# Optimization experiments

Measured on AMD Instinct MI355X. Metric: run time of the kernel, lower is better.

## Reference

```python
import jax, jax.numpy as jnp
import numpy as np
from jax import lax

# dims
BATCH, SEQ, DMODEL = 2, 2048, 1024
EXPAND, HEADDIM, DSTATE, DCONV, MLP_INNER = 2, 64, 64, 4, 4096
DIN = EXPAND * DMODEL            # 2048
NH = DIN // HEADDIM              # 32 heads
CONV_DIM = DIN + 2 * DSTATE      # x, B, C go through the depthwise conv
DPROJ = 2 * DIN + 2 * DSTATE + NH  # z, xBC, dt
EPS = 1e-5


def rmsnorm(x, w):
    return x * lax.rsqrt(jnp.mean(x * x, axis=-1, keepdims=True) + EPS) * w


def setup_inputs() -> dict:
    key = jax.random.key(0)
    ks = jax.random.split(key, 12)
    n = lambda i, shape, scale: jax.random.normal(ks[i], shape, jnp.float32) * scale
    return {
        "hidden_tokens": n(0, (BATCH, SEQ, DMODEL), 1.0),
        "W_in": n(1, (DMODEL, DPROJ), DMODEL ** -0.5),
        "conv_w": n(2, (CONV_DIM, DCONV), 0.2),
        "conv_b": jnp.zeros((CONV_DIM,), jnp.float32),
        "dt_bias": jax.random.uniform(ks[3], (NH,), jnp.float32, -4.0, -1.0),
        "A_log": jnp.log(jax.random.uniform(ks[4], (NH,), jnp.float32, 1.0, 16.0)),
        "D_param": n(5, (NH,), 1.0),
        "norm_w": jnp.ones((DIN,), jnp.float32),
        "W_out": n(6, (DIN, DMODEL), DIN ** -0.5),
        "rms_w": jnp.ones((DMODEL,), jnp.float32),
        "mlp_w1": n(7, (DMODEL, MLP_INNER), DMODEL ** -0.5),
        "mlp_b1": jnp.zeros((MLP_INNER,), jnp.float32),
        "mlp_w2": n(8, (MLP_INNER, DMODEL), MLP_INNER ** -0.5),
        "mlp_b2": jnp.zeros((DMODEL,), jnp.float32),
    }


def _mamba2(x, W_in, conv_w, conv_b, dt_bias, A_log, D_param, norm_w, W_out):
    b, l, _ = x.shape
    zxbcdt = x @ W_in                                   # (b,l,DPROJ)
    z = zxbcdt[..., :DIN]
    xBC = zxbcdt[..., DIN:DIN + CONV_DIM]
    dt = zxbcdt[..., DIN + CONV_DIM:]                   # (b,l,NH)

    # depthwise causal conv1d over sequence
    xt = jnp.pad(xBC, ((0, 0), (DCONV - 1, 0), (0, 0))).transpose(0, 2, 1)  # (b,c,l+pad)
    conv = lax.conv_general_dilated(xt, conv_w[:, None, :], (1,), "VALID",
                                    feature_group_count=CONV_DIM,
                                    dimension_numbers=("NCH", "OIH", "NCH"))
    xBC = jax.nn.silu(conv.transpose(0, 2, 1) + conv_b)  # (b,l,CONV_DIM)

    xs = xBC[..., :DIN].reshape(b, l, NH, HEADDIM)       # (b,l,h,p)
    Bc = xBC[..., DIN:DIN + DSTATE]                      # (b,l,n), ngroups=1
    Cc = xBC[..., DIN + DSTATE:]                         # (b,l,n)

    dt = jax.nn.softplus(dt + dt_bias)                   # (b,l,h)
    A = -jnp.exp(A_log)                                  # (h,)
    dA = jnp.exp(dt * A)                                 # (b,l,h)
    dtx = dt[..., None] * xs                             # (b,l,h,p)

    def step(h, inp):
        dA_t, dtx_t, B_t, C_t = inp                      # (b,h),(b,h,p),(b,n),(b,n)
        h = dA_t[..., None, None] * h + dtx_t[..., None] * B_t[:, None, None, :]
        y = jnp.einsum("bhpn,bn->bhp", h, C_t)
        return h, y

    h0 = jnp.zeros((b, NH, HEADDIM, DSTATE), x.dtype)
    _, ys = lax.scan(step, h0, (dA.transpose(1, 0, 2), dtx.transpose(1, 0, 2, 3),
                                Bc.transpose(1, 0, 2), Cc.transpose(1, 0, 2)))
    y = ys.transpose(1, 0, 2, 3) + D_param[None, None, :, None] * xs  # (b,l,h,p)
    y = y.reshape(b, l, DIN)
    y = rmsnorm(y * jax.nn.silu(z), norm_w)              # gated RMSNorm
    return y @ W_out


def reference(hidden_tokens, W_in, conv_w, conv_b, dt_bias, A_log, D_param,
              norm_w, W_out, rms_w, mlp_w1, mlp_b1, mlp_w2, mlp_b2):
    h = hidden_tokens + _mamba2(hidden_tokens, W_in, conv_w, conv_b, dt_bias,
                                A_log, D_param, norm_w, W_out)
    hn = rmsnorm(h, rms_w)
    mlp = jax.nn.silu(hn @ mlp_w1 + mlp_b1) @ mlp_w2 + mlp_b2
    return h + mlp
```

## Files before the change

kernel.cpp:

```cpp
#include <hip/hip_runtime.h>
#include <hip/hip_bf16.h>
#include <cstdint>
#include <cstddef>

#define BATCH 2
#define SEQ 2048
#define DMODEL 1024
#define DIN 2048
#define NH 32
#define HEADDIM 64
#define DSTATE 64
#define DCONV 4
#define CONV_DIM (DIN + 2 * DSTATE)
#define DPROJ (2 * DIN + 2 * DSTATE + NH)
#define MLP_INNER 4096
#define TOKENS (BATCH * SEQ)
#define EPS 1e-5f
#define Q 64
#define NCHUNK (SEQ / Q)
#define NCH (BATCH * NCHUNK * NH)
#define LSTR 72
#define NPAD_IN 4352

typedef __attribute__((ext_vector_type(8))) short short8;
typedef __attribute__((ext_vector_type(8))) __bf16 bf16x8;
typedef __attribute__((ext_vector_type(4))) float f32x4;

__device__ inline short f2bf(float f) {
    unsigned u = __builtin_bit_cast(unsigned, f);
    u = (u + 0x7FFFu + ((u >> 16) & 1u)) >> 16;
    return (short)u;
}
__device__ inline float bf2f(short s) {
    unsigned u = ((unsigned)(unsigned short)s) << 16;
    return __builtin_bit_cast(float, u);
}
__device__ inline float silu_f(float x) { return x / (1.f + __expf(-x)); }

__device__ inline bf16x8 ld_frag(const short* p) {
    short8 s = *(const short8*)p;
    return __builtin_bit_cast(bf16x8, s);
}

__device__ inline void glds16(const short* g, short* l) {
    __builtin_amdgcn_global_load_lds(
        (const __attribute__((address_space(1))) void*)g,
        (__attribute__((address_space(3))) void*)l, 16, 0, 0);
}

template <int MODE>
__global__ __launch_bounds__(512, 2) void gemm256_kernel(
    const short* __restrict__ A, const short* __restrict__ BT,
    void* __restrict__ Cout, const float* __restrict__ bias,
    int M, int N, int K)
{
    const int tid  = threadIdx.x;
    const int wid  = tid >> 6;
    const int lane = tid & 63;
    const int lm   = lane & 15;
    const int lg   = lane >> 4;
    const int wm   = (wid >> 2) * 128;
    const int wn   = (wid & 3) * 64;

    const int nb  = gridDim.x * gridDim.y;
    const int bid = blockIdx.y * gridDim.x + blockIdx.x;
    const int per = nb >> 3;
    const int nid = (bid & 7) * per + (bid >> 3);
    const int m0  = (nid / gridDim.x) * 256;
    const int n0  = (nid % gridDim.x) * 256;

    __shared__ __attribute__((aligned(16))) short Ab[2][2][256 * 32];
    __shared__ __attribute__((aligned(16))) short Bb[2][2][256 * 32];

    f32x4 acc[8][4];
#pragma unroll
    for (int i = 0; i < 8; ++i)
#pragma unroll
        for (int j = 0; j < 4; ++j) acc[i][j] = {0.f, 0.f, 0.f, 0.f};

    const int q   = tid & 7;
    const int jj  = (tid >> 3) & 3;
    const int win = tid >> 5;
    const int r0  = win * 8 + q;
    const short* Asrc = A  + (size_t)(m0 + r0) * K + jj * 8;
    const short* Bsrc = BT + (size_t)(n0 + r0) * K + jj * 8;
    const size_t rstep = (size_t)128 * K;
    const int dst = wid * 512;

#define STAGE(src, buf) do {                  \
        glds16((src), (buf) + dst);           \
        glds16((src) + rstep, (buf) + 4096 + dst); } while (0)

    bf16x8 af[8], bfr[4];

#define READ_A(As, i0, i1) do {                                                \
        _Pragma("unroll")                                                      \
        for (int fi = (i0); fi < (i1); ++fi) {                                 \
            int rr = wm + fi * 16 + lm;                                        \
            af[fi] = ld_frag((As) + ((rr >> 3) << 8) + ((rr & 7) << 3) + (lg << 6)); \
        }                                                                      \
    } while (0)

#define READ_B(Bs, j0, j1) do {                                                \
        _Pragma("unroll")                                                      \
        for (int fj = (j0); fj < (j1); ++fj) {                                 \
            int rr = wn + fj * 16 + lm;                                        \
            bfr[fj] = ld_frag((Bs) + ((rr >> 3) << 8) + ((rr & 7) << 3) + (lg << 6)); \
        }                                                                      \
    } while (0)

#define MFMAP(FJA) do {                                                        \
        __builtin_amdgcn_s_setprio(1);                                         \
        _Pragma("unroll")                                                      \
        for (int fi = 0; fi < 8; ++fi) {                                       \
            acc[fi][FJA]     = __builtin_amdgcn_mfma_f32_16x16x32_bf16(af[fi], bfr[FJA],     acc[fi][FJA],     0, 0, 0); \
            acc[fi][FJA + 1] = __builtin_amdgcn_mfma_f32_16x16x32_bf16(af[fi], bfr[FJA + 1], acc[fi][FJA + 1], 0, 0, 0); \
        }                                                                      \
        __builtin_amdgcn_s_setprio(0); } while (0)

#define BAR()      asm volatile("s_barrier" ::: "memory")
#define VM4_BAR()  asm volatile("s_waitcnt vmcnt(4)\n\ts_barrier" ::: "memory")
#define VM0_BAR()  asm volatile("s_waitcnt vmcnt(0)\n\ts_barrier" ::: "memory")
#define LGKM0()    asm volatile("s_waitcnt lgkmcnt(0)" ::: "memory")

    const int NT = K >> 6;

    STAGE(Asrc,      &Ab[0][0][0]);
    STAGE(Bsrc,      &Bb[0][0][0]);
    STAGE(Asrc + 32, &Ab[0][1][0]);
    STAGE(Bsrc + 32, &Bb[0][1][0]);
    VM4_BAR();
    READ_A(&Ab[0][0][0], 0, 4);

    for (int t = 0; t < NT - 1; ++t) {
        const int bi = t & 1, bn = bi ^ 1;
        const int kn = (t + 1) << 6;
        const short* A0c = &Ab[bi][0][0];
        const short* B0c = &Bb[bi][0][0];
        const short* A1c = &Ab[bi][1][0];
        const short* B1c = &Bb[bi][1][0];
        READ_A(A0c, 4, 8); READ_B(B0c, 0, 2);
        STAGE(Asrc + kn, &Ab[bn][0][0]);
        BAR(); LGKM0();
        MFMAP(0);
        READ_B(B0c, 2, 4);
        STAGE(Bsrc + kn, &Bb[bn][0][0]);
        VM4_BAR(); LGKM0();
        MFMAP(2);
        READ_A(A1c, 0, 4);
        READ_A(A1c, 4, 8); READ_B(B1c, 0, 2);
        STAGE(Asrc + kn + 32, &Ab[bn][1][0]);
        BAR(); LGKM0();
        MFMAP(0);
        READ_B(B1c, 2, 4);
        STAGE(Bsrc + kn + 32, &Bb[bn][1][0]);
        VM4_BAR(); LGKM0();
        MFMAP(2);
        READ_A(&Ab[bn][0][0], 0, 4);
    }
    {
        const int bi = (NT - 1) & 1;
        const short* A0c = &Ab[bi][0][0];
        const short* B0c = &Bb[bi][0][0];
        const short* A1c = &Ab[bi][1][0];
        const short* B1c = &Bb[bi][1][0];
        READ_A(A0c, 4, 8); READ_B(B0c, 0, 2);
        BAR(); LGKM0();
        MFMAP(0);
        READ_B(B0c, 2, 4);
        VM0_BAR(); LGKM0();
        MFMAP(2);
        READ_A(A1c, 0, 4);
        READ_A(A1c, 4, 8); READ_B(B1c, 0, 2);
        BAR(); LGKM0();
        MFMAP(0);
        READ_B(B1c, 2, 4);
        BAR(); LGKM0();
        MFMAP(2);
    }
#undef STAGE
#undef READ_A
#undef READ_B
#undef MFMAP
#undef BAR
#undef VM4_BAR
#undef VM0_BAR
#undef LGKM0

#pragma unroll
    for (int fj = 0; fj < 4; ++fj) {
        int col = n0 + wn + fj * 16 + lm;
        if (col < N) {
            float bv = (MODE == 1) ? bias[col] : 0.f;
#pragma unroll
            for (int fi = 0; fi < 8; ++fi) {
#pragma unroll
                for (int r = 0; r < 4; ++r) {
                    int row = m0 + wm + fi * 16 + lg * 4 + r;
                    float v = acc[fi][fj][r];
                    if (MODE == 1) v = silu_f(v + bv);
                    ((short*)Cout)[(size_t)row * N + col] = f2bf(v);
                }
            }
        }
    }
}

template <int MODE, int KT>
__global__ __launch_bounds__(256, (KT == 32) ? 4 : 2) void gemm_bf16_kernel(
    const short* __restrict__ A, const short* __restrict__ BT,
    void* __restrict__ Cout, const float* __restrict__ bias,
    const float* __restrict__ res, int M, int N, int K)
{
    const int tid  = threadIdx.x;
    const int wid  = tid >> 6;
    const int lane = tid & 63;
    const int lm   = lane & 15;
    const int lg   = lane >> 4;

    const int nb  = gridDim.x * gridDim.y;
    const int bid = blockIdx.y * gridDim.x + blockIdx.x;
    const int per = nb >> 3;
    const int nid = (bid & 7) * per + (bid >> 3);
    const int m0  = (nid / gridDim.x) * 128;
    const int n0  = (nid % gridDim.x) * 128;

    __shared__ __attribute__((aligned(16))) short Al0[128 * KT];
    __shared__ __attribute__((aligned(16))) short Al1[128 * KT];
    __shared__ __attribute__((aligned(16))) short Bl0[128 * KT];
    __shared__ __attribute__((aligned(16))) short Bl1[128 * KT];

    f32x4 acc[4][4];
#pragma unroll
    for (int i = 0; i < 4; ++i)
#pragma unroll
        for (int j = 0; j < 4; ++j) acc[i][j] = {0.f, 0.f, 0.f, 0.f};

    const int wm = (wid >> 1) * 64;
    const int wn = (wid & 1) * 64;

    constexpr int lpr = KT / 8;
    constexpr int rpi = 64 / lpr;
    constexpr int nin = 32 / rpi;
    const int srow = lane / lpr;
    const int scb  = (lane % lpr) ^ (srow & (lpr - 1));
    const int scol = scb * 8;
    const short* Ag = A  + (size_t)(m0 + wid * 32 + srow) * K + scol;
    const short* Bg = BT + (size_t)(n0 + wid * 32 + srow) * K + scol;
    const int woff = wid * 32 * KT;

    const int niter = K / KT;
    {
#pragma unroll
        for (int j = 0; j < nin; ++j) {
            glds16(Ag + (size_t)j * rpi * K, Al0 + woff + j * 512);
            glds16(Bg + (size_t)j * rpi * K, Bl0 + woff + j * 512);
        }
    }

    for (int i = 0; i < niter; ++i) {
        __syncthreads();
        const short* Ac = (i & 1) ? Al1 : Al0;
        const short* Bc = (i & 1) ? Bl1 : Bl0;
        if (i + 1 < niter) {
            int kt = (i + 1) * KT;
            short* al = ((i & 1) ? Al0 : Al1) + woff;
            short* bl = ((i & 1) ? Bl0 : Bl1) + woff;
#pragma unroll
            for (int j = 0; j < nin; ++j) {
                glds16(Ag + kt + (size_t)j * rpi * K, al + j * 512);
                glds16(Bg + kt + (size_t)j * rpi * K, bl + j * 512);
            }
        }

#pragma unroll
        for (int sub = 0; sub < KT / 32; ++sub) {
            const int cb = sub * 4 + lg;
            bf16x8 af[4], bf[4];
#pragma unroll
            for (int ii = 0; ii < 4; ++ii) {
                int ar = wm + ii * 16 + lm;
                af[ii] = ld_frag(&Ac[ar * KT + ((cb ^ (ar & (lpr - 1))) * 8)]);
            }
#pragma unroll
            for (int j = 0; j < 4; ++j) {
                int br = wn + j * 16 + lm;
                bf[j] = ld_frag(&Bc[br * KT + ((cb ^ (br & (lpr - 1))) * 8)]);
            }
#pragma unroll
            for (int ii = 0; ii < 4; ++ii)
#pragma unroll
                for (int j = 0; j < 4; ++j)
                    acc[ii][j] = __builtin_amdgcn_mfma_f32_16x16x32_bf16(af[ii], bf[j], acc[ii][j], 0, 0, 0);
        }
    }

#pragma unroll
    for (int i = 0; i < 4; ++i) {
#pragma unroll
        for (int j = 0; j < 4; ++j) {
            int col = n0 + wn + j * 16 + lm;
            if (col >= N) continue;
            float bv = (MODE == 1 || MODE == 2) ? bias[col] : 0.f;
#pragma unroll
            for (int r = 0; r < 4; ++r) {
                int row = m0 + wm + i * 16 + lg * 4 + r;
                float v = acc[i][j][r];
                if (MODE == 1) {
                    ((short*)Cout)[(size_t)row * N + col] = f2bf(silu_f(v + bv));
                } else if (MODE == 4) {
                    ((short*)Cout)[(size_t)row * N + col] = f2bf(v);
                } else {
                    if (MODE == 2) v = v + bv + res[(size_t)row * N + col];
                    if (MODE == 3) v = v + res[(size_t)row * N + col];
                    ((float*)Cout)[(size_t)row * N + col] = v;
                }
            }
        }
    }
}

__global__ __launch_bounds__(256) void cvt_kernel(
    const float* __restrict__ src, short* __restrict__ dst, int n4)
{
    int i = (blockIdx.x * 256 + threadIdx.x);
    if (i >= n4) return;
    f32x4 v = *(const f32x4*)(src + (size_t)i * 4);
    short4 o;
    o.x = f2bf(v.x); o.y = f2bf(v.y); o.z = f2bf(v.z); o.w = f2bf(v.w);
    *(short4*)(dst + (size_t)i * 4) = o;
}

__global__ __launch_bounds__(256) void transpose_kernel(
    const float* __restrict__ src, short* __restrict__ dst, int K, int N)
{
    __shared__ float t[32][33];
    int bx = blockIdx.x, by = blockIdx.y;
    int col = threadIdx.x & 31, row8 = threadIdx.x >> 5;
    int gn = bx * 32 + col;
#pragma unroll
    for (int r = 0; r < 4; ++r) {
        int gk = by * 32 + row8 + r * 8;
        t[row8 + r * 8][col] = (gn < N) ? src[(size_t)gk * N + gn] : 0.f;
    }
    __syncthreads();
#pragma unroll
    for (int r = 0; r < 4; ++r) {
        int n = bx * 32 + row8 + r * 8;
        dst[(size_t)n * K + by * 32 + col] = f2bf(t[col][row8 + r * 8]);
    }
}

#define CTOK 8
__global__ __launch_bounds__(256) void conv_kernel(
    const short* __restrict__ zx, const float* __restrict__ cw,
    const float* __restrict__ cb, short* __restrict__ xBCc)
{
    int c4 = blockIdx.y * 256 + threadIdx.x;
    if (c4 >= CONV_DIM / 4) return;
    int c  = c4 * 4;
    int m0 = blockIdx.x * CTOK;
    int l0 = m0 & (SEQ - 1);

    const short* base = zx + (size_t)m0 * DPROJ + DIN + c;
    f32x4 win[CTOK + 3];
#pragma unroll
    for (int j = 0; j < CTOK + 3; ++j) {
        int off = j - 3;
        if (l0 + off >= 0) {
            short4 sv = *(const short4*)(base + (ptrdiff_t)off * DPROJ);
            win[j] = {bf2f(sv.x), bf2f(sv.y), bf2f(sv.z), bf2f(sv.w)};
        } else {
            win[j] = {0.f, 0.f, 0.f, 0.f};
        }
    }
    f32x4 w0 = *(const f32x4*)(cw + (c + 0) * DCONV);
    f32x4 w1 = *(const f32x4*)(cw + (c + 1) * DCONV);
    f32x4 w2 = *(const f32x4*)(cw + (c + 2) * DCONV);
    f32x4 w3 = *(const f32x4*)(cw + (c + 3) * DCONV);
    f32x4 bb = *(const f32x4*)(cb + c);

    short* outp = xBCc + (size_t)m0 * CONV_DIM + c;
#pragma unroll
    for (int t = 0; t < CTOK; ++t) {
        f32x4 a = {bb.x, bb.y, bb.z, bb.w};
#pragma unroll
        for (int j = 0; j < DCONV; ++j) {
            f32x4 v = win[t + j];
            a.x += v.x * w0[j];
            a.y += v.y * w1[j];
            a.z += v.z * w2[j];
            a.w += v.w * w3[j];
        }
        short4 o;
        o.x = f2bf(silu_f(a.x)); o.y = f2bf(silu_f(a.y));
        o.z = f2bf(silu_f(a.z)); o.w = f2bf(silu_f(a.w));
        *(short4*)(outp + (size_t)t * CONV_DIM) = o;
    }
}

__global__ __launch_bounds__(256) void dt_kernel(
    const short* __restrict__ zx, const float* __restrict__ dt_bias,
    const float* __restrict__ A_log, float* __restrict__ dtb, float* __restrict__ ldab)
{
    int idx = blockIdx.x * 256 + threadIdx.x;
    if (idx >= TOKENS * NH) return;
    int hh = idx & (NH - 1);
    int m  = idx >> 5;
    float v  = bf2f(zx[(size_t)m * DPROJ + DIN + CONV_DIM + hh]) + dt_bias[hh];
    float dt = (v > 20.f) ? v : log1pf(__expf(v));
    dtb[idx]  = dt;
    ldab[idx] = -__expf(A_log[hh]) * dt;
}

__global__ __launch_bounds__(256) void chunk_kernel(
    const short* __restrict__ xBCc, const float* __restrict__ dtb,
    const float* __restrict__ ldab, float* __restrict__ ybuf,
    float* __restrict__ Sbuf, float* __restrict__ cumdecay)
{
    int bid = blockIdx.x;
    int h = bid & 31, c = (bid >> 5) & 31, b = bid >> 10;
    int m0 = b * SEQ + c * Q;
    int tid = threadIdx.x;
    int wid = tid >> 6, lane = tid & 63, lm = lane & 15, lg = lane >> 4;

    __shared__ __attribute__((aligned(16))) short Cc[64 * LSTR];
    __shared__ __attribute__((aligned(16))) short Bb[64 * LSTR];
    __shared__ __attribute__((aligned(16))) short BwT[64 * LSTR];
    __shared__ __attribute__((aligned(16))) short Xt[64 * LSTR];
    __shared__ __attribute__((aligned(16))) short Mm[64 * LSTR];
    __shared__ float Lc[64], dtv[64];

    if (tid < 64) {
        int s = tid;
        size_t ix = (size_t)(m0 + s) * NH + h;
        float ld = ldab[ix];
        float dt = dtb[ix];
        float v = ld;
#pragma unroll
        for (int off = 1; off < 64; off <<= 1) {
            float o = __shfl_up(v, off);
            if (s >= off) v += o;
        }
        Lc[s] = v;
        dtv[s] = dt;
        cumdecay[(size_t)bid * 64 + s] = __expf(v);
    }
    {
        int row = tid >> 2, c0 = (tid & 3) * 16;
        const short* pB = xBCc + (size_t)(m0 + row) * CONV_DIM + DIN;
#pragma unroll
        for (int u = 0; u < 2; ++u) {
            short8 vb = *(const short8*)(pB + c0 + 8 * u);
            short8 vc = *(const short8*)(pB + DSTATE + c0 + 8 * u);
            *(short8*)&Bb[row * LSTR + c0 + 8 * u] = vb;
            *(short8*)&Cc[row * LSTR + c0 + 8 * u] = vc;
        }
    }
    __syncthreads();
    {
        int s = tid >> 2, c0 = (tid & 3) * 16;
        float w = dtv[s];
        float w2 = __expf(Lc[63] - Lc[s]);
        const short* pX = xBCc + (size_t)(m0 + s) * CONV_DIM + h * HEADDIM;
#pragma unroll
        for (int u = 0; u < 4; ++u) {
            short4 v = *(const short4*)(pX + c0 + 4 * u);
            Xt[(c0 + 4 * u + 0) * LSTR + s] = f2bf(bf2f(v.x) * w);
            Xt[(c0 + 4 * u + 1) * LSTR + s] = f2bf(bf2f(v.y) * w);
            Xt[(c0 + 4 * u + 2) * LSTR + s] = f2bf(bf2f(v.z) * w);
            Xt[(c0 + 4 * u + 3) * LSTR + s] = f2bf(bf2f(v.w) * w);
            short4 sb = *(short4*)&Bb[s * LSTR + c0 + 4 * u];
            BwT[(c0 + 4 * u + 0) * LSTR + s] = f2bf(bf2f(sb.x) * w2);
            BwT[(c0 + 4 * u + 1) * LSTR + s] = f2bf(bf2f(sb.y) * w2);
            BwT[(c0 + 4 * u + 2) * LSTR + s] = f2bf(bf2f(sb.z) * w2);
            BwT[(c0 + 4 * u + 3) * LSTR + s] = f2bf(bf2f(sb.w) * w2);
        }
    }
    __syncthreads();

    {
        bf16x8 af[2];
#pragma unroll
        for (int kk = 0; kk < 2; ++kk)
            af[kk] = ld_frag(&Cc[(wid * 16 + lm) * LSTR + kk * 32 + lg * 8]);
#pragma unroll
        for (int j = 0; j < 4; ++j) {
            f32x4 acc = {0.f, 0.f, 0.f, 0.f};
#pragma unroll
            for (int kk = 0; kk < 2; ++kk) {
                bf16x8 bf = ld_frag(&Bb[(j * 16 + lm) * LSTR + kk * 32 + lg * 8]);
                acc = __builtin_amdgcn_mfma_f32_16x16x32_bf16(af[kk], bf, acc, 0, 0, 0);
            }
            int s = j * 16 + lm;
            float Ls = Lc[s];
#pragma unroll
            for (int r = 0; r < 4; ++r) {
                int t = wid * 16 + lg * 4 + r;
                float val = (s <= t) ? acc[r] * __expf(Lc[t] - Ls) : 0.f;
                Mm[t * LSTR + s] = f2bf(val);
            }
        }
    }
    __syncthreads();

    {
        bf16x8 am[2], aw[2];
#pragma unroll
        for (int kk = 0; kk < 2; ++kk) {
            am[kk] = ld_frag(&Mm[(wid * 16 + lm) * LSTR + kk * 32 + lg * 8]);
            aw[kk] = ld_frag(&BwT[(wid * 16 + lm) * LSTR + kk * 32 + lg * 8]);
        }
#pragma unroll
        for (int j = 0; j < 4; ++j) {
            f32x4 a1 = {0.f, 0.f, 0.f, 0.f};
            f32x4 a2 = {0.f, 0.f, 0.f, 0.f};
#pragma unroll
            for (int kk = 0; kk < 2; ++kk) {
                bf16x8 bx = ld_frag(&Xt[(j * 16 + lm) * LSTR + kk * 32 + lg * 8]);
                a1 = __builtin_amdgcn_mfma_f32_16x16x32_bf16(am[kk], bx, a1, 0, 0, 0);
                a2 = __builtin_amdgcn_mfma_f32_16x16x32_bf16(aw[kk], bx, a2, 0, 0, 0);
            }
            int p = j * 16 + lm;
#pragma unroll
            for (int r = 0; r < 4; ++r) {
                int t = wid * 16 + lg * 4 + r;
                ybuf[(size_t)(m0 + t) * DIN + h * HEADDIM + p] = a1[r];
                Sbuf[(size_t)bid * 4096 + t * 64 + p] = a2[r];
            }
        }
    }
}

__global__ __launch_bounds__(256) void state_kernel(
    float* __restrict__ SH, const float* __restrict__ cumdecay)
{
    int bh = blockIdx.x;
    int b = bh >> 5, h = bh & 31;
    int tid = threadIdx.x;
    f32x4 H[4];
#pragma unroll
    for (int u = 0; u < 4; ++u) H[u] = {0.f, 0.f, 0.f, 0.f};
    for (int c = 0; c < NCHUNK; ++c) {
        int cid = (b * NCHUNK + c) * NH + h;
        size_t base = (size_t)cid * 4096 + (size_t)tid * 16;
        float cd = cumdecay[(size_t)cid * 64 + 63];
        f32x4 s[4];
#pragma unroll
        for (int u = 0; u < 4; ++u) s[u] = *(const f32x4*)(SH + base + u * 4);
#pragma unroll
        for (int u = 0; u < 4; ++u) *(f32x4*)(SH + base + u * 4) = H[u];
#pragma unroll
        for (int u = 0; u < 4; ++u) {
            H[u].x = cd * H[u].x + s[u].x;
            H[u].y = cd * H[u].y + s[u].y;
            H[u].z = cd * H[u].z + s[u].z;
            H[u].w = cd * H[u].w + s[u].w;
        }
    }
}

__global__ __launch_bounds__(256) void inter_kernel(
    const short* __restrict__ xBCc, const float* __restrict__ Hin,
    const float* __restrict__ cumdecay, float* __restrict__ ybuf)
{
    int bid = blockIdx.x;
    int h = bid & 31, c = (bid >> 5) & 31, b = bid >> 10;
    int m0 = b * SEQ + c * Q;
    int tid = threadIdx.x;
    int wid = tid >> 6, lane = tid & 63, lm = lane & 15, lg = lane >> 4;

    __shared__ __attribute__((aligned(16))) short Cc[64 * LSTR];
    __shared__ __attribute__((aligned(16))) short HT[64 * LSTR];
    __shared__ float eLc[64];

    if (tid < 64) eLc[tid] = cumdecay[(size_t)bid * 64 + tid];
    {
        int row = tid >> 2, c0 = (tid & 3) * 16;
        const short* pC = xBCc + (size_t)(m0 + row) * CONV_DIM + DIN + DSTATE;
#pragma unroll
        for (int u = 0; u < 2; ++u) {
            short8 vc = *(const short8*)(pC + c0 + 8 * u);
            *(short8*)&Cc[row * LSTR + c0 + 8 * u] = vc;
        }
        const float* pH = Hin + (size_t)bid * 4096 + row * 64;
#pragma unroll
        for (int u = 0; u < 4; ++u) {
            f32x4 vh = *(const f32x4*)(pH + c0 + 4 * u);
            HT[(c0 + 4 * u + 0) * LSTR + row] = f2bf(vh.x);
            HT[(c0 + 4 * u + 1) * LSTR + row] = f2bf(vh.y);
            HT[(c0 + 4 * u + 2) * LSTR + row] = f2bf(vh.z);
            HT[(c0 + 4 * u + 3) * LSTR + row] = f2bf(vh.w);
        }
    }
    __syncthreads();

    bf16x8 af[2];
#pragma unroll
    for (int kk = 0; kk < 2; ++kk)
        af[kk] = ld_frag(&Cc[(wid * 16 + lm) * LSTR + kk * 32 + lg * 8]);
#pragma unroll
    for (int j = 0; j < 4; ++j) {
        f32x4 acc = {0.f, 0.f, 0.f, 0.f};
#pragma unroll
        for (int kk = 0; kk < 2; ++kk) {
            bf16x8 bh_ = ld_frag(&HT[(j * 16 + lm) * LSTR + kk * 32 + lg * 8]);
            acc = __builtin_amdgcn_mfma_f32_16x16x32_bf16(af[kk], bh_, acc, 0, 0, 0);
        }
        int p = j * 16 + lm;
#pragma unroll
        for (int r = 0; r < 4; ++r) {
            int t = wid * 16 + lg * 4 + r;
            size_t ya = (size_t)(m0 + t) * DIN + h * HEADDIM + p;
            ybuf[ya] += eLc[t] * acc[r];
        }
    }
}

__global__ __launch_bounds__(256) void norm1_kernel(
    const short* __restrict__ zx, const short* __restrict__ xBCc,
    const float* __restrict__ Dp, const float* __restrict__ y,
    short* __restrict__ ybf, const float* __restrict__ w)
{
    int m = blockIdx.x;
    int t = threadIdx.x;
    const short* zr = zx + (size_t)m * DPROJ;
    const short* xr = xBCc + (size_t)m * CONV_DIM;
    const float* yr = y + (size_t)m * DIN;
    float vals[8];
    float ss = 0.f;
#pragma unroll
    for (int j = 0; j < 8; ++j) {
        int i = j * 256 + t;
        float v = (yr[i] + Dp[i >> 6] * bf2f(xr[i])) * silu_f(bf2f(zr[i]));
        vals[j] = v;
        ss += v * v;
    }
#pragma unroll
    for (int o = 32; o >= 1; o >>= 1) ss += __shfl_xor(ss, o);
    __shared__ float wsum[4];
    if ((t & 63) == 0) wsum[t >> 6] = ss;
    __syncthreads();
    float tot = wsum[0] + wsum[1] + wsum[2] + wsum[3];
    float scale = rsqrtf(tot / (float)DIN + EPS);
#pragma unroll
    for (int j = 0; j < 8; ++j) {
        int i = j * 256 + t;
        ybf[(size_t)m * DIN + i] = f2bf(vals[j] * scale * w[i]);
    }
}

__global__ __launch_bounds__(256) void norm2_kernel(
    const float* __restrict__ hb, short* __restrict__ hnbf, const float* __restrict__ w)
{
    int m = blockIdx.x;
    int t = threadIdx.x;
    const float* hr = hb + (size_t)m * DMODEL;
    float vals[4];
    float ss = 0.f;
#pragma unroll
    for (int j = 0; j < 4; ++j) {
        int i = j * 256 + t;
        float v = hr[i];
        vals[j] = v;
        ss += v * v;
    }
#pragma unroll
    for (int o = 32; o >= 1; o >>= 1) ss += __shfl_xor(ss, o);
    __shared__ float wsum[4];
    if ((t & 63) == 0) wsum[t >> 6] = ss;
    __syncthreads();
    float tot = wsum[0] + wsum[1] + wsum[2] + wsum[3];
    float scale = rsqrtf(tot / (float)DMODEL + EPS);
#pragma unroll
    for (int j = 0; j < 4; ++j) {
        int i = j * 256 + t;
        hnbf[(size_t)m * DMODEL + i] = f2bf(vals[j] * scale * w[i]);
    }
}

extern "C" void kernel_launch(void* const* d_in, const int* in_sizes, int n_in,
                              void* d_out, int out_size, void* d_ws, size_t ws_size,
                              hipStream_t stream) {
    const float* x       = (const float*)d_in[0];
    const float* W_in    = (const float*)d_in[1];
    const float* conv_w  = (const float*)d_in[2];
    const float* conv_b  = (const float*)d_in[3];
    const float* dt_bias = (const float*)d_in[4];
    const float* A_log   = (const float*)d_in[5];
    const float* D_param = (const float*)d_in[6];
    const float* norm_w  = (const float*)d_in[7];
    const float* W_out   = (const float*)d_in[8];
    const float* rms_w   = (const float*)d_in[9];
    const float* mlp_w1  = (const float*)d_in[10];
    const float* mlp_b1  = (const float*)d_in[11];
    const float* mlp_w2  = (const float*)d_in[12];
    const float* mlp_b2  = (const float*)d_in[13];
    float* out = (float*)d_out;

    float* ws       = (float*)d_ws;
    float* zxf      = ws;
    float* xBCf     = zxf + (size_t)TOKENS * DPROJ;
    float* dtb      = xBCf + (size_t)TOKENS * CONV_DIM;
    float* ldab     = dtb + (size_t)TOKENS * NH;
    float* cumdecay = ldab + (size_t)TOKENS * NH;
    float* ybuf     = cumdecay + (size_t)TOKENS * NH;
    float* SH       = ybuf + (size_t)TOKENS * DIN;
    float* bfarea   = SH + (size_t)NCH * 4096;

    short* zxb   = (short*)zxf;
    short* xBCb  = (short*)xBCf;
    short* xbf   = (short*)ybuf;
    short* midbf = (short*)ybuf;
    float* hbuf  = SH;
    short* hnbf  = (short*)(SH + (size_t)TOKENS * DMODEL);

    short* ybf   = (short*)bfarea;
    short* WinT  = ybf + (size_t)TOKENS * DIN;
    short* WoutT = WinT + (size_t)NPAD_IN * DMODEL;
    short* w1T   = WoutT + (size_t)DMODEL * DIN;
    short* w2T   = w1T + (size_t)MLP_INNER * DMODEL;

    dim3 blk(256);
    dim3 blk2(512);

    cvt_kernel<<<dim3(TOKENS * DMODEL / 4 / 256), blk, 0, stream>>>(x, xbf, TOKENS * DMODEL / 4);
    transpose_kernel<<<dim3(NPAD_IN / 32, DMODEL / 32), blk, 0, stream>>>(W_in, WinT, DMODEL, DPROJ);
    transpose_kernel<<<dim3(DMODEL / 32, DIN / 32), blk, 0, stream>>>(W_out, WoutT, DIN, DMODEL);
    transpose_kernel<<<dim3(MLP_INNER / 32, DMODEL / 32), blk, 0, stream>>>(mlp_w1, w1T, DMODEL, MLP_INNER);
    transpose_kernel<<<dim3(DMODEL / 32, MLP_INNER / 32), blk, 0, stream>>>(mlp_w2, w2T, MLP_INNER, DMODEL);

    gemm_bf16_kernel<4, 32><<<dim3(NPAD_IN / 128, TOKENS / 128), blk, 0, stream>>>(
        xbf, WinT, zxb, nullptr, nullptr, TOKENS, DPROJ, DMODEL);
    conv_kernel<<<dim3(TOKENS / CTOK, (CONV_DIM / 4 + 255) / 256), blk, 0, stream>>>(
        zxb, conv_w, conv_b, xBCb);
    dt_kernel<<<dim3(TOKENS * NH / 256), blk, 0, stream>>>(zxb, dt_bias, A_log, dtb, ldab);
    chunk_kernel<<<dim3(NCH), blk, 0, stream>>>(xBCb, dtb, ldab, ybuf, SH, cumdecay);
    state_kernel<<<dim3(BATCH * NH), blk, 0, stream>>>(SH, cumdecay);
    inter_kernel<<<dim3(NCH), blk, 0, stream>>>(xBCb, SH, cumdecay, ybuf);
    norm1_kernel<<<dim3(TOKENS), blk, 0, stream>>>(zxb, xBCb, D_param, ybuf, ybf, norm_w);
    gemm_bf16_kernel<3, 64><<<dim3(DMODEL / 128, TOKENS / 128), blk, 0, stream>>>(
        ybf, WoutT, hbuf, nullptr, x, TOKENS, DMODEL, DIN);
    norm2_kernel<<<dim3(TOKENS), blk, 0, stream>>>(hbuf, hnbf, rms_w);
    gemm256_kernel<1><<<dim3(MLP_INNER / 256, TOKENS / 256), blk2, 0, stream>>>(
        hnbf, w1T, midbf, mlp_b1, TOKENS, MLP_INNER, DMODEL);
    gemm_bf16_kernel<2, 64><<<dim3(DMODEL / 128, TOKENS / 128), blk, 0, stream>>>(
        midbf, w2T, out, mlp_b2, hbuf, TOKENS, DMODEL, MLP_INNER);
}
```

Measured before the change: 421.7 us.

## Use 64x128 GEMM tiles for N=1024 GEMMs and split state scan across blocks

Adds a 64x128-tile bf16 MFMA GEMM with double-buffered LDS, XOR-swizzled layout and an XCD-aware block remap. It replaces the 128x128 GEMM for the out-projection and the second MLP GEMM. With N=1024 the old tiling launched only 256 blocks, and the smaller tiles double the block count to fill the CUs better, at the cost of more re-reads of B per output. The inter-chunk state scan is also split four ways per (batch, head), and the next chunk's load is prefetched, giving the serial recurrence more parallelism and hiding its load latency.

Result: faster. 407.6 us (-3.3%).

```diff
diff --git a/kernel.cpp b/kernel.cpp
--- a/kernel.cpp
+++ b/kernel.cpp
@@ -320,6 +320,109 @@
     }
 }
 
+template <int MODE>
+__global__ __launch_bounds__(256, 2) void gemm64_kernel(
+    const short* __restrict__ A, const short* __restrict__ BT,
+    float* __restrict__ Cout, const float* __restrict__ bias,
+    const float* __restrict__ res, int M, int N, int K)
+{
+    constexpr int KT = 64;
+    const int tid  = threadIdx.x;
+    const int wid  = tid >> 6;
+    const int lane = tid & 63;
+    const int lm   = lane & 15;
+    const int lg   = lane >> 4;
+    const int wn   = wid * 32;
+
+    const int nb  = gridDim.x * gridDim.y;
+    const int bid = blockIdx.y * gridDim.x + blockIdx.x;
+    const int per = nb >> 3;
+    const int nid = (bid & 7) * per + (bid >> 3);
+    const int m0  = (nid / gridDim.x) * 64;
+    const int n0  = (nid % gridDim.x) * 128;
+
+    __shared__ __attribute__((aligned(16))) short Al0[64 * KT];
+    __shared__ __attribute__((aligned(16))) short Al1[64 * KT];
+    __shared__ __attribute__((aligned(16))) short Bl0[128 * KT];
+    __shared__ __attribute__((aligned(16))) short Bl1[128 * KT];
+
+    f32x4 acc[4][2];
+#pragma unroll
+    for (int i = 0; i < 4; ++i)
+#pragma unroll
+        for (int j = 0; j < 2; ++j) acc[i][j] = {0.f, 0.f, 0.f, 0.f};
+
+    const int srow = lane >> 3;
+    const int scb  = (lane & 7) ^ (srow & 7);
+    const int scol = scb * 8;
+    const short* Bg = BT + (size_t)(n0 + wid * 32 + srow) * K + scol;
+    const short* Ag = A  + (size_t)(m0 + (wid & 1) * 32 + srow) * K + scol;
+    const int woffB = wid * 32 * KT;
+    const int woffA = (wid & 1) * 32 * KT;
+    const bool doA = (wid < 2);
+
+    const int niter = K / KT;
+    {
+#pragma unroll
+        for (int j = 0; j < 4; ++j) {
+            if (doA) glds16(Ag + (size_t)j * 8 * K, Al0 + woffA + j * 512);
+            glds16(Bg + (size_t)j * 8 * K, Bl0 + woffB + j * 512);
+        }
+    }
+
+    for (int i = 0; i < niter; ++i) {
+        __syncthreads();
+        const short* Ac = (i & 1) ? Al1 : Al0;
+        const short* Bc = (i & 1) ? Bl1 : Bl0;
+        if (i + 1 < niter) {
+            int kt = (i + 1) * KT;
+            short* al = ((i & 1) ? Al0 : Al1) + woffA;
+            short* bl = ((i & 1) ? Bl0 : Bl1) + woffB;
+#pragma unroll
+            for (int j = 0; j < 4; ++j) {
+                if (doA) glds16(Ag + kt + (size_t)j * 8 * K, al + j * 512);
+                glds16(Bg + kt + (size_t)j * 8 * K, bl + j * 512);
+            }
+        }
+
+#pragma unroll
+        for (int sub = 0; sub < 2; ++sub) {
+            const int cb = sub * 4 + lg;
+            bf16x8 af[4], bf[2];
+#pragma unroll
+            for (int ii = 0; ii < 4; ++ii) {
+                int ar = ii * 16 + lm;
+                af[ii] = ld_frag(&Ac[ar * KT + ((cb ^ (ar & 7)) * 8)]);
+            }
+#pragma unroll
+            for (int j = 0; j < 2; ++j) {
+                int br = wn + j * 16 + lm;
+                bf[j] = ld_frag(&Bc[br * KT + ((cb ^ (br & 7)) * 8)]);
+            }
+#pragma unroll
+            for (int ii = 0; ii < 4; ++ii)
+#pragma unroll
+                for (int j = 0; j < 2; ++j)
+                    acc[ii][j] = __builtin_amdgcn_mfma_f32_16x16x32_bf16(af[ii], bf[j], acc[ii][j], 0, 0, 0);
+        }
+    }
+
+#pragma unroll
+    for (int j = 0; j < 2; ++j) {
+        int col = n0 + wn + j * 16 + lm;
+        float bv = (MODE == 2) ? bias[col] : 0.f;
+#pragma unroll
+        for (int i = 0; i < 4; ++i) {
+#pragma unroll
+            for (int r = 0; r < 4; ++r) {
+                int row = m0 + i * 16 + lg * 4 + r;
+                float v = acc[i][j][r] + bv + res[(size_t)row * N + col];
+                Cout[(size_t)row * N + col] = v;
+            }
+        }
+    }
+}
+
 __global__ __launch_bounds__(256) void cvt_kernel(
     const float* __restrict__ src, short* __restrict__ dst, int n4)
 {
@@ -535,28 +638,30 @@
 __global__ __launch_bounds__(256) void state_kernel(
     float* __restrict__ SH, const float* __restrict__ cumdecay)
 {
-    int bh = blockIdx.x;
+    int bh = blockIdx.x >> 2, st = blockIdx.x & 3;
     int b = bh >> 5, h = bh & 31;
-    int tid = threadIdx.x;
-    f32x4 H[4];
-#pragma unroll
-    for (int u = 0; u < 4; ++u) H[u] = {0.f, 0.f, 0.f, 0.f};
+    size_t off = (size_t)st * 1024 + (size_t)threadIdx.x * 4;
+
+    f32x4 H = {0.f, 0.f, 0.f, 0.f};
+    int cid = b * NCHUNK * NH + h;
+    f32x4 s_next = *(const f32x4*)(SH + (size_t)cid * 4096 + off);
+    float cd_next = cumdecay[(size_t)cid * 64 + 63];
+
     for (int c = 0; c < NCHUNK; ++c) {
-        int cid = (b * NCHUNK + c) * NH + h;
-        size_t base = (size_t)cid * 4096 + (size_t)tid * 16;
-        float cd = cumdecay[(size_t)cid * 64 + 63];
-        f32x4 s[4];
-#pragma unroll
-        for (int u = 0; u < 4; ++u) s[u] = *(const f32x4*)(SH + base + u * 4);
-#pragma unroll
-        for (int u = 0; u < 4; ++u) *(f32x4*)(SH + base + u * 4) = H[u];
-#pragma unroll
-        for (int u = 0; u < 4; ++u) {
-            H[u].x = cd * H[u].x + s[u].x;
-            H[u].y = cd * H[u].y + s[u].y;
-            H[u].z = cd * H[u].z + s[u].z;
-            H[u].w = cd * H[u].w + s[u].w;
-        }
+        f32x4 s = s_next;
+        float cd = cd_next;
+        size_t base = (size_t)cid * 4096 + off;
+        if (c + 1 < NCHUNK) {
+            int cid1 = cid + NH;
+            s_next = *(const f32x4*)(SH + (size_t)cid1 * 4096 + off);
+            cd_next = cumdecay[(size_t)cid1 * 64 + 63];
+        }
+        *(f32x4*)(SH + base) = H;
+        H.x = cd * H.x + s.x;
+        H.y = cd * H.y + s.y;
+        H.z = cd * H.z + s.z;
+        H.w = cd * H.w + s.w;
+        cid += NH;
     }
 }
 
@@ -736,14 +841,14 @@
         zxb, conv_w, conv_b, xBCb);
     dt_kernel<<<dim3(TOKENS * NH / 256), blk, 0, stream>>>(zxb, dt_bias, A_log, dtb, ldab);
     chunk_kernel<<<dim3(NCH), blk, 0, stream>>>(xBCb, dtb, ldab, ybuf, SH, cumdecay);
-    state_kernel<<<dim3(BATCH * NH), blk, 0, stream>>>(SH, cumdecay);
+    state_kernel<<<dim3(BATCH * NH * 4), blk, 0, stream>>>(SH, cumdecay);
     inter_kernel<<<dim3(NCH), blk, 0, stream>>>(xBCb, SH, cumdecay, ybuf);
     norm1_kernel<<<dim3(TOKENS), blk, 0, stream>>>(zxb, xBCb, D_param, ybuf, ybf, norm_w);
-    gemm_bf16_kernel<3, 64><<<dim3(DMODEL / 128, TOKENS / 128), blk, 0, stream>>>(
+    gemm64_kernel<3><<<dim3(DMODEL / 128, TOKENS / 64), blk, 0, stream>>>(
         ybf, WoutT, hbuf, nullptr, x, TOKENS, DMODEL, DIN);
     norm2_kernel<<<dim3(TOKENS), blk, 0, stream>>>(hbuf, hnbf, rms_w);
     gemm256_kernel<1><<<dim3(MLP_INNER / 256, TOKENS / 256), blk2, 0, stream>>>(
         hnbf, w1T, midbf, mlp_b1, TOKENS, MLP_INNER, DMODEL);
-    gemm_bf16_kernel<2, 64><<<dim3(DMODEL / 128, TOKENS / 128), blk, 0, stream>>>(
+    gemm64_kernel<2><<<dim3(DMODEL / 128, TOKENS / 64), blk, 0, stream>>>(
         midbf, w2T, out, mlp_b2, hbuf, TOKENS, DMODEL, MLP_INNER);
 }
```
